# Kernel tuning notes

Measured on AMD Instinct MI355X. Metric: run time of the kernel, lower is better.

The kernel has to match this reference:

```python
import jax, jax.numpy as jnp
import numpy as np

B, N, F_IN = 256, 256, 128
HID, DEPTH = 48, 4
D_OUT = 97                 # sum(latent_dim [32,32,32,1]) = GraphUNet out_channels
K_SORT = 30
C1, C2, KW2 = 16, 32, 5
POOL_LEN = (K_SORT - 2) // 2 + 1        # 15 after maxpool1d(2,2)
DENSE_DIM = (POOL_LEN - KW2 + 1) * C2   # 352
OUT_DIM = 32


def _gcn(x, A, W, b):
    # GCNConv(improved=True): A_hat = A + 2I; out = D^-1/2 A_hat D^-1/2 (x W) + b
    n = A.shape[-1]
    Ah = A + 2.0 * jnp.eye(n, dtype=A.dtype)
    dinv = jax.lax.rsqrt(jnp.sum(Ah, axis=-1))          # deg >= 2 always
    An = dinv[:, :, None] * Ah * dinv[:, None, :]
    return An @ (x @ W) + b


def _augment(A):
    # GraphUNet.augment_adj: add self loops, two-hop (A@A), remove self loops
    n = A.shape[-1]
    eye = jnp.eye(n, dtype=A.dtype)
    A1 = A + eye
    return (A1 @ A1) * (1.0 - eye)


def _topk_pool(x, A, p):
    # TopKPooling(ratio=0.5, nonlinearity=tanh): score = tanh(x.p/||p||)
    Bb, n, _ = x.shape
    score = jnp.tanh((x @ p) / jnp.sqrt(jnp.sum(p * p)))
    k = (n + 1) // 2
    vals, perm = jax.lax.top_k(score, k)                # [B,k]
    bidx = jnp.arange(Bb)[:, None]
    xp = x[bidx, perm] * vals[..., None]                # gate kept nodes by score
    Ap = A[bidx[..., None], perm[:, :, None], perm[:, None, :]]
    return xp, Ap, perm


def _forward(x, A, dW0, db0, dW, db, pool_p, uW, ub, uWl, ubl, c1W, c1b, c2W, c2b, oW, ob):
    act = jax.nn.relu
    # ---- GraphUNet down path ----
    h = act(_gcn(x, A, dW0, db0))
    xs, As, perms = [h], [A], []
    Acur = A
    for i in range(DEPTH):
        A2 = _augment(Acur)
        h, Acur, perm = _topk_pool(h, A2, pool_p[i])
        h = act(_gcn(h, Acur, dW[i], db[i]))
        if i < DEPTH - 1:
            xs.append(h)
            As.append(Acur)
        perms.append(perm)
    # ---- up path with sum skip connections ----
    for i in range(DEPTH):
        j = DEPTH - 1 - i
        res, Aj, perm = xs[j], As[j], perms[j]
        bidx = jnp.arange(res.shape[0])[:, None]
        up = jnp.zeros_like(res).at[bidx, perm].set(h)
        h = res + up
        if i < DEPTH - 1:
            h = act(_gcn(h, Aj, uW[i], ub[i]))
        else:
            h = _gcn(h, Aj, uWl, ubl)                   # [B,N,D_OUT], no act
    # ---- global_sort_pool: sort nodes by last channel desc, keep top K_SORT ----
    _, order = jax.lax.top_k(h[..., -1], K_SORT)
    sp = h[jnp.arange(B)[:, None], order]               # [B,K_SORT,D_OUT]
    # conv1d(1->C1, kernel=stride=D_OUT) on flattened [B,1,K*D] == per-node linear
    y = jax.nn.relu(jnp.einsum('bkd,cd->bck', sp, c1W) + c1b[None, :, None])  # [B,C1,K]
    y = y.reshape(B, C1, POOL_LEN, 2).max(-1)           # maxpool1d(2,2)
    y = jax.lax.conv_general_dilated(y, c2W, (1,), 'VALID',
                                     dimension_numbers=('NCH', 'OIH', 'NCH'))
    y = jax.nn.relu(y + c2b[None, :, None])             # [B,C2,POOL_LEN-KW2+1]
    return jax.nn.relu(y.reshape(B, -1) @ oW + ob)      # relu(relu(.)) == relu(.)


def setup_inputs():
    key = jax.random.key(0)
    ks = jax.random.split(key, 12)
    x = jax.random.normal(ks[0], (B, N, F_IN), dtype=jnp.float32)
    # symmetric binary adjacency, no self loops, avg degree ~15
    u = jax.random.uniform(ks[1], (B, N, N))
    A = (u < 0.03).astype(jnp.float32)
    A = jnp.maximum(A, A.transpose(0, 2, 1)) * (1.0 - jnp.eye(N, dtype=jnp.float32))
    s = lambda f: np.float32(1.0 / np.sqrt(f))
    return dict(
        x=x, A=A,
        dW0=jax.random.normal(ks[2], (F_IN, HID), dtype=jnp.float32) * s(F_IN),
        db0=jnp.zeros((HID,), jnp.float32),
        dW=jax.random.normal(ks[3], (DEPTH, HID, HID), dtype=jnp.float32) * s(HID),
        db=jnp.zeros((DEPTH, HID), jnp.float32),
        pool_p=jax.random.normal(ks[4], (DEPTH, HID), dtype=jnp.float32) * s(HID),
        uW=jax.random.normal(ks[5], (DEPTH - 1, HID, HID), dtype=jnp.float32) * s(HID),
        ub=jnp.zeros((DEPTH - 1, HID), jnp.float32),
        uWl=jax.random.normal(ks[6], (HID, D_OUT), dtype=jnp.float32) * s(HID),
        ubl=jnp.zeros((D_OUT,), jnp.float32),
        c1W=jax.random.normal(ks[7], (C1, D_OUT), dtype=jnp.float32) * s(D_OUT),
        c1b=jnp.zeros((C1,), jnp.float32),
        c2W=jax.random.normal(ks[8], (C2, C1, KW2), dtype=jnp.float32) * s(C1 * KW2),
        c2b=jnp.zeros((C2,), jnp.float32),
        oW=jax.random.normal(ks[9], (DENSE_DIM, OUT_DIM), dtype=jnp.float32) * s(DENSE_DIM),
        ob=jnp.zeros((OUT_DIM,), jnp.float32),
    )


def reference(x, A, dW0, db0, dW, db, pool_p, uW, ub, uWl, ubl, c1W, c1b, c2W, c2b, oW, ob):
    return _forward(x, A, dW0, db0, dW, db, pool_p, uW, ub, uWl, ubl, c1W, c1b, c2W, c2b, oW, ob)
```

## Files before the change

### kernel.cpp

```cpp
#include <hip/hip_runtime.h>
#include <math.h>

#define BATCH 256
#define NNODE 256
#define FIN   128
#define HID   48
#define DOUT  97

#define WOFF_DW0 0
#define WOFF_DW  6144
#define WOFF_UW  18432
#define WOFF_UWL 27648
#define WTOT     34816

typedef __attribute__((ext_vector_type(8))) short bf16x8_t;
typedef __attribute__((ext_vector_type(4))) float f32x4_t;

__device__ inline unsigned short f2bf(float x) {
  unsigned u = __float_as_uint(x);
  u += 0x7fff + ((u >> 16) & 1);
  return (unsigned short)(u >> 16);
}
__device__ inline float bf2f(unsigned short h) {
  return __uint_as_float(((unsigned)h) << 16);
}

template<int L> __device__ inline float grp_sum(float v) {
  #pragma unroll
  for (int o = L >> 1; o > 0; o >>= 1) v += __shfl_xor(v, o);
  return v;
}
template<int L> __device__ inline int grp_isum(int v) {
  #pragma unroll
  for (int o = L >> 1; o > 0; o >>= 1) v += __shfl_xor(v, o);
  return v;
}

__global__ __launch_bounds__(256) void k_prepA(const float* __restrict__ A,
                                               unsigned short* __restrict__ Abf,
                                               float* __restrict__ dinv, int rows) {
  int wid = (blockIdx.x * 256 + threadIdx.x) >> 6;
  int lane = threadIdx.x & 63;
  if (wid >= rows) return;
  const float4* rp = (const float4*)(A + (size_t)wid * 256);
  float4 v = rp[lane];
  unsigned long long pk = (unsigned long long)f2bf(v.x)
                        | ((unsigned long long)f2bf(v.y) << 16)
                        | ((unsigned long long)f2bf(v.z) << 32)
                        | ((unsigned long long)f2bf(v.w) << 48);
  *(unsigned long long*)(Abf + (size_t)wid * 256 + lane * 4) = pk;
  float s = v.x + v.y + v.z + v.w;
  #pragma unroll
  for (int o = 32; o > 0; o >>= 1) s += __shfl_down(s, o);
  if (lane == 0) dinv[wid] = 1.0f / sqrtf(s + 2.0f);
}

__global__ __launch_bounds__(256) void k_dinv_bf(const unsigned short* __restrict__ Abf,
                                                 float* __restrict__ dinv, int n, int rows) {
  int wid = (blockIdx.x * 256 + threadIdx.x) >> 6;
  int lane = threadIdx.x & 63;
  if (wid >= rows) return;
  const unsigned short* row = Abf + (size_t)wid * n;
  float s = 0.f;
  for (int j = lane * 2; j < n; j += 128) {
    unsigned u = *(const unsigned*)(row + j);
    s += bf2f((unsigned short)(u & 0xffffu)) + bf2f((unsigned short)(u >> 16));
  }
  #pragma unroll
  for (int o = 32; o > 0; o >>= 1) s += __shfl_down(s, o);
  if (lane == 0) dinv[wid] = 1.0f / sqrtf(s + 2.0f);
}

__global__ __launch_bounds__(256) void k_splitW3(const float* __restrict__ dW0,
                                                 const float* __restrict__ dW,
                                                 const float* __restrict__ uW,
                                                 const float* __restrict__ uWl,
                                                 unsigned short* __restrict__ Wp) {
  int idx = blockIdx.x * 256 + threadIdx.x;
  if (idx >= WTOT) return;
  float v;
  if (idx < WOFF_DW) {
    int f = idx / 128, kk = idx - f * 128;
    v = dW0[kk * HID + f];
  } else if (idx < WOFF_UW) {
    int r = idx - WOFF_DW;
    int i = r / 3072; r -= i * 3072;
    int f = r / 64, kk = r - f * 64;
    v = (kk < HID) ? dW[((size_t)i * HID + kk) * HID + f] : 0.f;
  } else if (idx < WOFF_UWL) {
    int r = idx - WOFF_UW;
    int i = r / 3072; r -= i * 3072;
    int f = r / 64, kk = r - f * 64;
    v = (kk < HID) ? uW[((size_t)i * HID + kk) * HID + f] : 0.f;
  } else {
    int r = idx - WOFF_UWL;
    int f = r / 64, kk = r - f * 64;
    v = (f < DOUT && kk < HID) ? uWl[(size_t)kk * DOUT + f] : 0.f;
  }
  unsigned short h = f2bf(v);
  float r1 = v - bf2f(h);
  unsigned short m = f2bf(r1);
  float r2 = r1 - bf2f(m);
  unsigned short l = f2bf(r2);
  Wp[idx] = h;
  Wp[idx + WTOT] = m;
  Wp[idx + 2 * WTOT] = l;
}

template<int KS2>
__global__ __launch_bounds__(256) void k_xws(const float* __restrict__ X,
                                             const unsigned short* __restrict__ Wp,
                                             float* __restrict__ XW,
                                             const float* __restrict__ dinv,
                                             unsigned short* __restrict__ Yth,
                                             unsigned short* __restrict__ Ytl,
                                             int K, int F, int Fpad, int nShift) {
  constexpr int KP = KS2 * 32;
  int mt = (blockIdx.x * 256 + threadIdx.x) >> 6;
  int lane = threadIdx.x & 63;
  int r = lane & 15, q = lane >> 4;
  const float* xr = X + ((long)mt * 16 + r) * K;
  bf16x8_t ah[KS2], am[KS2], al[KS2];
  #pragma unroll
  for (int ks = 0; ks < KS2; ks++) {
    int col0 = ks * 32 + q * 8;
    float v[8];
    if (col0 + 8 <= K) {
      float4 a = *(const float4*)(xr + col0);
      float4 b = *(const float4*)(xr + col0 + 4);
      v[0] = a.x; v[1] = a.y; v[2] = a.z; v[3] = a.w;
      v[4] = b.x; v[5] = b.y; v[6] = b.z; v[7] = b.w;
    } else {
      #pragma unroll
      for (int j = 0; j < 8; j++) v[j] = (col0 + j < K) ? xr[col0 + j] : 0.f;
    }
    #pragma unroll
    for (int j = 0; j < 8; j++) {
      unsigned short h = f2bf(v[j]);
      float r1 = v[j] - bf2f(h);
      unsigned short m = f2bf(r1);
      float r2 = r1 - bf2f(m);
      unsigned short l = f2bf(r2);
      ah[ks][j] = (short)h;
      am[ks][j] = (short)m;
      al[ks][j] = (short)l;
    }
  }
  long row0 = (long)mt * 16 + q * 4;
  float4 dv4 = {0.f, 0.f, 0.f, 0.f};
  long ytBase = 0;
  if (Yth) {
    dv4 = *(const float4*)(dinv + row0);
    int bb = (int)(row0 >> nShift);
    int jj = (int)(row0 & ((1 << nShift) - 1));
    ytBase = (long)bb * Fpad;
    ytBase = ytBase << nShift;
    ytBase += jj;
  }
  int nFT = Fpad >> 4;
  for (int ft = 0; ft < nFT; ft++) {
    int fl = ft * 16 + r;
    const unsigned short* wb = Wp + (size_t)fl * KP + q * 8;
    f32x4_t acc = {0.f, 0.f, 0.f, 0.f};
    #pragma unroll
    for (int ks = 0; ks < KS2; ks++) {
      bf16x8_t bh = *(const bf16x8_t*)(wb + ks * 32);
      bf16x8_t bm = *(const bf16x8_t*)(wb + WTOT + ks * 32);
      bf16x8_t bl = *(const bf16x8_t*)(wb + 2 * WTOT + ks * 32);
      acc = __builtin_amdgcn_mfma_f32_16x16x32_bf16(ah[ks], bh, acc, 0, 0, 0);
      acc = __builtin_amdgcn_mfma_f32_16x16x32_bf16(ah[ks], bm, acc, 0, 0, 0);
      acc = __builtin_amdgcn_mfma_f32_16x16x32_bf16(am[ks], bh, acc, 0, 0, 0);
      acc = __builtin_amdgcn_mfma_f32_16x16x32_bf16(am[ks], bm, acc, 0, 0, 0);
      acc = __builtin_amdgcn_mfma_f32_16x16x32_bf16(ah[ks], bl, acc, 0, 0, 0);
      acc = __builtin_amdgcn_mfma_f32_16x16x32_bf16(al[ks], bh, acc, 0, 0, 0);
    }
    int f = fl;
    if (f < F) {
      if (XW) {
        #pragma unroll
        for (int reg = 0; reg < 4; reg++) XW[(row0 + reg) * F + f] = acc[reg];
      }
      if (Yth) {
        float dvv[4] = {dv4.x, dv4.y, dv4.z, dv4.w};
        unsigned long long hpk = 0, lpk = 0;
        #pragma unroll
        for (int reg = 0; reg < 4; reg++) {
          float v = dvv[reg] * acc[reg];
          unsigned short hi = f2bf(v);
          unsigned short lo = f2bf(v - bf2f(hi));
          hpk |= ((unsigned long long)hi) << (16 * reg);
          lpk |= ((unsigned long long)lo) << (16 * reg);
        }
        long o = ytBase + ((long)f << nShift);
        *(unsigned long long*)(Yth + o) = hpk;
        *(unsigned long long*)(Ytl + o) = lpk;
      }
    }
  }
}

template<int KS, int ITP>
__global__ __launch_bounds__(256) void k_gcn2(
    const unsigned short* __restrict__ Abf, const float* __restrict__ dinv,
    const unsigned short* __restrict__ Yth, const unsigned short* __restrict__ Ytl,
    const float* __restrict__ bias, float* __restrict__ out,
    int F, int Fpad, int dorelu) {
  constexpr int n = KS * 32;
  int b = blockIdx.x & (BATCH - 1);
  int sub = blockIdx.x >> 8;
  int wave = threadIdx.x >> 6, lane = threadIdx.x & 63;
  int r = lane & 15, q = lane >> 4;
  const float* dv = dinv + (size_t)b * n;
  int itBase = (sub * 4 + wave) * ITP;
  bf16x8_t af[ITP][KS];
  #pragma unroll
  for (int l = 0; l < ITP; l++) {
    const unsigned short* ap = Abf + ((size_t)b * n + (itBase + l) * 16 + r) * n + q * 8;
    #pragma unroll
    for (int ks = 0; ks < KS; ks++) af[l][ks] = *(const bf16x8_t*)(ap + ks * 32);
  }
  float di[ITP][4];
  #pragma unroll
  for (int l = 0; l < ITP; l++) {
    int i0 = (itBase + l) * 16 + q * 4;
    #pragma unroll
    for (int reg = 0; reg < 4; reg++) di[l][reg] = dv[i0 + reg];
  }
  int nFT = Fpad >> 4;
  for (int ft = 0; ft < nFT; ft++) {
    int fl = ft * 16 + r;
    const unsigned short* yrowh = Yth + ((size_t)b * Fpad + fl) * n;
    const unsigned short* yrowl = Ytl + ((size_t)b * Fpad + fl) * n;
    f32x4_t acc[ITP];
    #pragma unroll
    for (int l = 0; l < ITP; l++) acc[l] = (f32x4_t){0.f, 0.f, 0.f, 0.f};
    #pragma unroll
    for (int ks = 0; ks < KS; ks++) {
      bf16x8_t bh = *(const bf16x8_t*)(yrowh + q * 8 + ks * 32);
      bf16x8_t bl = *(const bf16x8_t*)(yrowl + q * 8 + ks * 32);
      #pragma unroll
      for (int l = 0; l < ITP; l++) {
        acc[l] = __builtin_amdgcn_mfma_f32_16x16x32_bf16(af[l][ks], bh, acc[l], 0, 0, 0);
        acc[l] = __builtin_amdgcn_mfma_f32_16x16x32_bf16(af[l][ks], bl, acc[l], 0, 0, 0);
      }
    }
    if (fl < F) {
      float bf = bias[fl];
      #pragma unroll
      for (int l = 0; l < ITP; l++) {
        int i0 = (itBase + l) * 16 + q * 4;
        unsigned long long hq = *(const unsigned long long*)(yrowh + i0);
        unsigned long long lq = *(const unsigned long long*)(yrowl + i0);
        #pragma unroll
        for (int reg = 0; reg < 4; reg++) {
          float yv = bf2f((unsigned short)(hq >> (16 * reg)))
                   + bf2f((unsigned short)(lq >> (16 * reg)));
          float v = di[l][reg] * acc[l][reg] + 2.f * di[l][reg] * yv + bf;
          if (dorelu) v = fmaxf(v, 0.f);
          out[((size_t)b * n + i0 + reg) * F + fl] = v;
        }
      }
    }
  }
}

__global__ __launch_bounds__(512) void k_htail(const unsigned short* __restrict__ Abf,
                                               const float* __restrict__ dinv,
                                               const unsigned short* __restrict__ Yth,
                                               const unsigned short* __restrict__ Ytl,
                                               const float* __restrict__ ubl,
                                               float* __restrict__ sp) {
  int b = blockIdx.x, t = threadIdx.x;
  __shared__ float sy[256];
  __shared__ float sc[256];
  __shared__ int sord[32];
  const unsigned short* yh = Yth + ((size_t)b * 112 + 96) * 256;
  const unsigned short* yl = Ytl + ((size_t)b * 112 + 96) * 256;
  if (t < 256) sy[t] = bf2f(yh[t]) + bf2f(yl[t]);
  __syncthreads();
  {
    int i = t >> 1, sub = t & 1;
    const unsigned short* ar = Abf + ((size_t)b * 256 + i) * 256 + sub * 128;
    const float* syp = sy + sub * 128;
    float s = 0.f;
    for (int j = 0; j < 128; j += 2) {
      unsigned u = *(const unsigned*)(ar + j);
      s += bf2f((unsigned short)(u & 0xffffu)) * syp[j]
         + bf2f((unsigned short)(u >> 16)) * syp[j + 1];
    }
    s += __shfl_xor(s, 1);
    if (sub == 0) {
      float d = dinv[(size_t)b * 256 + i];
      sc[i] = d * s + 2.f * d * sy[i];
    }
  }
  __syncthreads();
  {
    int i = t >> 1, sub = t & 1;
    float v = sc[i];
    int r = 0;
    int j0 = sub * 128;
    for (int j = j0; j < j0 + 128; j++) {
      float u = sc[j];
      r += (u > v) || (u == v && j < i);
    }
    r += __shfl_xor(r, 1);
    if (sub == 0 && r < 30) sord[r] = i;
  }
  __syncthreads();
  int wave = t >> 6, lane = t & 63;
  int it = wave & 1, fh = wave >> 1;
  int r = lane & 15, q = lane >> 4;
  int ari = it * 16 + r;
  int arow = sord[ari < 30 ? ari : 0];
  const unsigned short* ap = Abf + ((size_t)b * 256 + arow) * 256 + q * 8;
  bf16x8_t af[8];
  #pragma unroll
  for (int ks = 0; ks < 8; ks++) af[ks] = *(const bf16x8_t*)(ap + ks * 32);
  int ftBeg = fh * 2, ftEnd = fh * 2 + 2;
  if (ftEnd > 7) ftEnd = 7;
  for (int ft = ftBeg; ft < ftEnd; ft++) {
    int fl = ft * 16 + r;
    const unsigned short* yrowh = Yth + ((size_t)b * 112 + fl) * 256;
    const unsigned short* yrowl = Ytl + ((size_t)b * 112 + fl) * 256;
    f32x4_t acc = {0.f, 0.f, 0.f, 0.f};
    #pragma unroll
    for (int ks = 0; ks < 8; ks++) {
      bf16x8_t bh = *(const bf16x8_t*)(yrowh + q * 8 + ks * 32);
      bf16x8_t bl = *(const bf16x8_t*)(yrowl + q * 8 + ks * 32);
      acc = __builtin_amdgcn_mfma_f32_16x16x32_bf16(af[ks], bh, acc, 0, 0, 0);
      acc = __builtin_amdgcn_mfma_f32_16x16x32_bf16(af[ks], bl, acc, 0, 0, 0);
    }
    if (fl < DOUT) {
      float bf = ubl[fl];
      #pragma unroll
      for (int reg = 0; reg < 4; reg++) {
        int rowidx = it * 16 + q * 4 + reg;
        if (rowidx < 30) {
          int node = sord[rowidx];
          float d = dinv[(size_t)b * 256 + node];
          float yv = bf2f(yrowh[node]) + bf2f(yrowl[node]);
          sp[((size_t)b * 30 + rowidx) * DOUT + fl] = d * acc[reg] + 2.f * d * yv + bf;
        }
      }
    }
  }
}

__global__ __launch_bounds__(256) void k_aug_mfma(const unsigned short* __restrict__ Abf,
                                                  const int* __restrict__ perm,
                                                  float* __restrict__ Ap,
                                                  unsigned short* __restrict__ Apbf,
                                                  int n, int k) {
  int kt = k >> 4;
  int inner = blockIdx.x & 255;
  int slot = blockIdx.x >> 8;
  int b = ((inner & 7) << 5) | (inner >> 3);
  int wave = threadIdx.x >> 6, lane = threadIdx.x & 63;
  int tile = slot * 4 + wave;
  int it = tile / kt, ft = tile - it * kt;
  int r = lane & 15, q = lane >> 4;
  const int* pm = perm + (size_t)b * k;
  int rowA = pm[it * 16 + r];
  int rowB = pm[ft * 16 + r];
  const unsigned short* Ab = Abf + (size_t)b * n * n;
  const unsigned short* pa = Ab + (size_t)rowA * n + q * 8;
  const unsigned short* pb = Ab + (size_t)rowB * n + q * 8;
  f32x4_t acc = {0.f, 0.f, 0.f, 0.f};
  for (int k0 = 0; k0 < n; k0 += 32) {
    bf16x8_t a  = *(const bf16x8_t*)(pa + k0);
    bf16x8_t bv = *(const bf16x8_t*)(pb + k0);
    int daA = rowA - k0 - q * 8;
    int daB = rowB - k0 - q * 8;
    #pragma unroll
    for (int e = 0; e < 8; e++) {
      if (daA == e) a[e] = (short)0x3F80;
      if (daB == e) bv[e] = (short)0x3F80;
    }
    acc = __builtin_amdgcn_mfma_f32_16x16x32_bf16(a, bv, acc, 0, 0, 0);
  }
  int c = ft * 16 + r;
  #pragma unroll
  for (int reg = 0; reg < 4; reg++) {
    int rr = it * 16 + q * 4 + reg;
    float v = acc[reg];
    if (rr == c) v = 0.f;
    if (Ap)   Ap[((size_t)b * k + rr) * k + c] = v;
    if (Apbf) Apbf[((size_t)b * k + rr) * k + c] = f2bf(v);
  }
}

__global__ __launch_bounds__(256) void k_pool(const float* __restrict__ H,
                                              const float* __restrict__ p,
                                              int* __restrict__ perm,
                                              float* __restrict__ Hout,
                                              int n, int k) {
  int b = blockIdx.x, t = threadIdx.x;
  __shared__ float s[256];
  __shared__ int sord[128];
  float pn = 0.f;
  #pragma unroll
  for (int j = 0; j < HID; j++) pn += p[j] * p[j];
  if (t < n) {
    const float* hr = H + ((size_t)b * n + t) * HID;
    float acc = 0.f;
    #pragma unroll
    for (int j = 0; j < HID; j++) acc += hr[j] * p[j];
    s[t] = tanhf(acc / sqrtf(pn));
  }
  __syncthreads();
  if (t < n) {
    float v = s[t];
    int r = 0;
    for (int j = 0; j < n; j++) {
      float u = s[j];
      r += (u > v) || (u == v && j < t);
    }
    if (r < k) { perm[(size_t)b * k + r] = t; sord[r] = t; }
  }
  __syncthreads();
  for (int idx = t; idx < k * HID; idx += 256) {
    int r = idx / HID, f = idx - r * HID;
    int pi = sord[r];
    Hout[((size_t)b * k + r) * HID + f] = H[((size_t)b * n + pi) * HID + f] * s[pi];
  }
}

__global__ __launch_bounds__(256) void k_scatter(const int* __restrict__ perm,
                                                 const float* __restrict__ Hsrc,
                                                 float* __restrict__ Hdst,
                                                 int n, int k, int total) {
  int idx = blockIdx.x * 256 + threadIdx.x;
  if (idx >= total) return;
  int f = idx % HID;
  int r = (idx / HID) % k;
  int b = idx / (HID * k);
  int pi = perm[(size_t)b * k + r];
  Hdst[((size_t)b * n + pi) * HID + f] += Hsrc[idx];
}

__global__ __launch_bounds__(256) void k_head2(const float* __restrict__ spg,
                                               const float* __restrict__ c1W,
                                               const float* __restrict__ c1b,
                                               const float* __restrict__ c2W,
                                               const float* __restrict__ c2b,
                                               const float* __restrict__ oW,
                                               const float* __restrict__ ob,
                                               float* __restrict__ out) {
  int b = blockIdx.x, t = threadIdx.x;
  __shared__ float sp[30 * 97];
  __shared__ float y1[16 * 30];
  __shared__ float yp[16 * 15];
  __shared__ float yc[32 * 11];
  const float* spb = spg + (size_t)b * 30 * 97;
  for (int idx = t; idx < 30 * 97; idx += 256) sp[idx] = spb[idx];
  __syncthreads();
  for (int idx = t; idx < 16 * 30; idx += 256) {
    int c = idx / 30, kk = idx - c * 30;
    float a = c1b[c];
    for (int d = 0; d < 97; d++) a += sp[kk * 97 + d] * c1W[c * 97 + d];
    y1[c * 30 + kk] = fmaxf(a, 0.f);
  }
  __syncthreads();
  for (int idx = t; idx < 16 * 15; idx += 256) {
    int c = idx / 15, t2 = idx - c * 15;
    yp[idx] = fmaxf(y1[c * 30 + 2 * t2], y1[c * 30 + 2 * t2 + 1]);
  }
  __syncthreads();
  for (int idx = t; idx < 32 * 11; idx += 256) {
    int o = idx / 11, t3 = idx - o * 11;
    float a = c2b[o];
    for (int i2 = 0; i2 < 16; i2++)
      for (int w = 0; w < 5; w++)
        a += yp[i2 * 15 + t3 + w] * c2W[(o * 16 + i2) * 5 + w];
    yc[o * 11 + t3] = fmaxf(a, 0.f);
  }
  __syncthreads();
  if (t < 32) {
    float a = ob[t];
    for (int q = 0; q < 352; q++) a += yc[q] * oW[q * 32 + t];
    out[(size_t)b * 32 + t] = fmaxf(a, 0.f);
  }
}


__device__ inline void xw_dphase(const float* hin, const float* W, const float* dv,
                                 float* xwd, int n, int t) {
  for (int idx = t; idx < n * 48; idx += 512) {
    int j = idx / 48, f = idx - j * 48;
    const float* hr = hin + j * 48;
    float a = 0.f;
    #pragma unroll
    for (int g = 0; g < 48; g++) a += hr[g] * W[g * 48 + f];
    xwd[idx] = dv[j] * a;
  }
}

__device__ inline void anxw_phase(const float* A, int lda, const float* xwd,
                                  const float* dv, const float* bias,
                                  float* hout, int n, int t) {
  for (int idx = t; idx < n * 48; idx += 512) {
    int i = idx / 48, f = idx - i * 48;
    const float* ar = A + i * lda;
    float acc = 0.f;
    #pragma unroll 4
    for (int j = 0; j < n; j++) acc += ar[j] * xwd[j * 48 + f];
    float di = dv[i];
    float v = di * acc + 2.f * di * xwd[i * 48 + f] + bias[f];
    hout[idx] = fmaxf(v, 0.f);
  }
}

template<int N, int K>
__device__ inline void pool_phaseT(const float* h, const float* p,
                                   float* sS, int* perm, float* hin, int t) {
  constexpr int LPR = 512 / N;
  int row = t / LPR, sub = t % LPR;
  float pn = 0.f;
  #pragma unroll
  for (int g = 0; g < 48; g++) pn += p[g] * p[g];
  const float* hr = h + row * 48;
  float acc = 0.f;
  for (int g = sub; g < 48; g += LPR) acc += hr[g] * p[g];
  acc = grp_sum<LPR>(acc);
  if (sub == 0) sS[row] = tanhf(acc / sqrtf(pn));
  __syncthreads();
  {
    float v = sS[row];
    int r = 0;
    for (int j = sub; j < N; j += LPR) {
      float u = sS[j];
      r += (u > v) || (u == v && j < row);
    }
    r = grp_isum<LPR>(r);
    if (sub == 0 && r < K) perm[r] = row;
  }
  __syncthreads();
  for (int idx = t; idx < K * 48; idx += 512) {
    int r = idx / 48, g = idx - r * 48;
    int pi = perm[r];
    hin[idx] = h[pi * 48 + g] * sS[pi];
  }
  __syncthreads();
}

template<int NN, int KK>
__device__ inline void aug_phaseT(const float* A, int lda, const int* perm,
                                  float* Ao, int ldo, float* dout, int t) {
  for (int idx = t; idx < KK * KK; idx += 512) {
    int r = idx / KK, c = idx - r * KK;
    int pr = perm[r], pc = perm[c];
    const float* ra = A + pr * lda;
    const float* rc = A + pc * lda;
    float acc = 0.f;
    #pragma unroll 4
    for (int j = 0; j < NN; j++) acc += ra[j] * rc[j];
    float v = acc + 2.f * ra[pc];
    Ao[r * ldo + c] = (r == c) ? 0.f : v;
  }
  __syncthreads();
  {
    constexpr int LPR = 512 / KK;
    int row = t / LPR, sub = t % LPR;
    float s = 0.f;
    for (int j = sub; j < KK; j += LPR) s += Ao[row * ldo + j];
    s = grp_sum<LPR>(s);
    if (sub == 0) dout[row] = 1.0f / sqrtf(s + 2.0f);
  }
  __syncthreads();
}

__device__ inline void scat_phase(const int* perm, const float* src, float* dst,
                                  int k, int t) {
  for (int idx = t; idx < k * 48; idx += 512) {
    int r = idx / 48, g = idx - r * 48;
    dst[perm[r] * 48 + g] += src[idx];
  }
  __syncthreads();
}

__global__ __launch_bounds__(512) void k_inner(const unsigned short* __restrict__ Abf1g,
                                               float* __restrict__ H1g,
                                               const float* __restrict__ dW,
                                               const float* __restrict__ dbv,
                                               const float* __restrict__ pp,
                                               const float* __restrict__ uW,
                                               const float* __restrict__ ub) {
  int b = blockIdx.x, t = threadIdx.x;
  const unsigned short* A1 = Abf1g + (size_t)b * 128 * 128;
  float* H1 = H1g + (size_t)b * 128 * 48;

  __shared__ float sS[128];
  __shared__ int   sP2[64], sP3[32], sP4[16];
  __shared__ float sD2[64], sD3[32], sD4[16];
  __shared__ float sA2[64 * 65];
  __shared__ float sA3[32 * 33];
  __shared__ float sH2[64 * 48];
  __shared__ float sH3[32 * 48];
  __shared__ float sU[6144];
  float* hin = sU;
  float* sXW = sU + 3072;
  float* sH4 = sU + 1536;
  float* sA4 = sU + 2304;

  {
    const float* p = pp + 48;
    float pn = 0.f;
    #pragma unroll
    for (int g = 0; g < 48; g++) pn += p[g] * p[g];
    int row = t >> 2, sub = t & 3;
    const float* hr = H1 + row * 48;
    float acc = 0.f;
    for (int g = sub; g < 48; g += 4) acc += hr[g] * p[g];
    acc = grp_sum<4>(acc);
    if (sub == 0) sS[row] = tanhf(acc / sqrtf(pn));
    __syncthreads();
    float v = sS[row];
    int rk = 0;
    for (int j = sub; j < 128; j += 4) {
      float u = sS[j];
      rk += (u > v) || (u == v && j < row);
    }
    rk = grp_isum<4>(rk);
    if (sub == 0 && rk < 64) sP2[rk] = row;
    __syncthreads();
  }

  {
    int wave = t >> 6, lane = t & 63;
    int r = lane & 15, q = lane >> 4;
    #pragma unroll
    for (int tt = 0; tt < 2; tt++) {
      int tile = wave * 2 + tt;
      int it = tile >> 2, ft = tile & 3;
      int rowA = sP2[it * 16 + r];
      int rowB = sP2[ft * 16 + r];
      const unsigned short* pa = A1 + (size_t)rowA * 128 + q * 8;
      const unsigned short* pb = A1 + (size_t)rowB * 128 + q * 8;
      f32x4_t acc = {0.f, 0.f, 0.f, 0.f};
      #pragma unroll
      for (int k0 = 0; k0 < 128; k0 += 32) {
        bf16x8_t a  = *(const bf16x8_t*)(pa + k0);
        bf16x8_t bv = *(const bf16x8_t*)(pb + k0);
        int daA = rowA - k0 - q * 8;
        int daB = rowB - k0 - q * 8;
        #pragma unroll
        for (int e = 0; e < 8; e++) {
          if (daA == e) a[e] = (short)0x3F80;
          if (daB == e) bv[e] = (short)0x3F80;
        }
        acc = __builtin_amdgcn_mfma_f32_16x16x32_bf16(a, bv, acc, 0, 0, 0);
      }
      int c = ft * 16 + r;
      #pragma unroll
      for (int reg = 0; reg < 4; reg++) {
        int rr = it * 16 + q * 4 + reg;
        sA2[rr * 65 + c] = (rr == c) ? 0.f : acc[reg];
      }
    }
    for (int idx = t; idx < 64 * 48; idx += 512) {
      int r2 = idx / 48, g = idx - r2 * 48;
      int pi = sP2[r2];
      hin[idx] = H1[pi * 48 + g] * sS[pi];
    }
  }
  __syncthreads();
  {
    int row = t >> 3, sub = t & 7;
    float s = 0.f;
    for (int j = sub; j < 64; j += 8) s += sA2[row * 65 + j];
    s = grp_sum<8>(s);
    if (sub == 0) sD2[row] = 1.0f / sqrtf(s + 2.0f);
  }
  __syncthreads();
  xw_dphase(hin, dW + 2304, sD2, sXW, 64, t);
  __syncthreads();
  anxw_phase(sA2, 65, sXW, sD2, dbv + 48, sH2, 64, t);
  __syncthreads();

  pool_phaseT<64, 32>(sH2, pp + 96, sS, sP3, hin, t);
  aug_phaseT<64, 32>(sA2, 65, sP3, sA3, 33, sD3, t);
  xw_dphase(hin, dW + 2 * 2304, sD3, sXW, 32, t);
  __syncthreads();
  anxw_phase(sA3, 33, sXW, sD3, dbv + 96, sH3, 32, t);
  __syncthreads();

  pool_phaseT<32, 16>(sH3, pp + 144, sS, sP4, hin, t);
  aug_phaseT<32, 16>(sA3, 33, sP4, sA4, 17, sD4, t);
  xw_dphase(hin, dW + 3 * 2304, sD4, sXW, 16, t);
  __syncthreads();
  anxw_phase(sA4, 17, sXW, sD4, dbv + 144, sH4, 16, t);
  __syncthreads();

  scat_phase(sP4, sH4, sH3, 16, t);
  xw_dphase(sH3, uW, sD3, sXW, 32, t);
  __syncthreads();
  anxw_phase(sA3, 33, sXW, sD3, ub, sH3, 32, t);
  __syncthreads();

  scat_phase(sP3, sH3, sH2, 32, t);
  xw_dphase(sH2, uW + 2304, sD2, sXW, 64, t);
  __syncthreads();
  anxw_phase(sA2, 65, sXW, sD2, ub + 48, sH2, 64, t);
  __syncthreads();

  for (int idx = t; idx < 64 * 48; idx += 512) {
    int r2 = idx / 48, g = idx - r2 * 48;
    H1[sP2[r2] * 48 + g] += sH2[idx];
  }
}

extern "C" void kernel_launch(void* const* d_in, const int* in_sizes, int n_in,
                              void* d_out, int out_size, void* d_ws, size_t ws_size,
                              hipStream_t stream) {
  const float* x   = (const float*)d_in[0];
  const float* A0  = (const float*)d_in[1];
  const float* dW0 = (const float*)d_in[2];
  const float* db0 = (const float*)d_in[3];
  const float* dW  = (const float*)d_in[4];
  const float* dbv = (const float*)d_in[5];
  const float* pp  = (const float*)d_in[6];
  const float* uW  = (const float*)d_in[7];
  const float* ub  = (const float*)d_in[8];
  const float* uWl = (const float*)d_in[9];
  const float* ubl = (const float*)d_in[10];
  const float* c1W = (const float*)d_in[11];
  const float* c1b = (const float*)d_in[12];
  const float* c2W = (const float*)d_in[13];
  const float* c2b = (const float*)d_in[14];
  const float* oW  = (const float*)d_in[15];
  const float* ob  = (const float*)d_in[16];
  float* out = (float*)d_out;

  float* base = (float*)d_ws;
  size_t off = 0;
  auto alloc = [&](size_t nel) { nel = (nel + 3) & ~(size_t)3; float* p = base + off; off += nel; return p; };
  float* H0 = alloc((size_t)BATCH * 256 * HID);
  float* H1 = alloc((size_t)BATCH * 128 * HID);
  float* D0 = alloc((size_t)BATCH * 256);
  float* D1 = alloc((size_t)BATCH * 128);
  float* SP  = alloc((size_t)BATCH * 30 * 97);
  int* P1 = (int*)alloc((size_t)BATCH * 128);
  unsigned short* Abf0 = (unsigned short*)alloc((size_t)BATCH * 256 * 256 / 2);
  unsigned short* Abf1 = (unsigned short*)alloc((size_t)BATCH * 128 * 128 / 2);
  unsigned short* Yth  = (unsigned short*)alloc((size_t)BATCH * 112 * 256 / 2);
  unsigned short* Ytl  = (unsigned short*)alloc((size_t)BATCH * 112 * 256 / 2);
  unsigned short* Wp   = (unsigned short*)alloc((size_t)3 * WTOT / 2 + 4);

  k_prepA<<<BATCH * 256 / 4, 256, 0, stream>>>(A0, Abf0, D0, BATCH * 256);
  k_splitW3<<<(WTOT + 255) / 256, 256, 0, stream>>>(dW0, dW, uW, uWl, Wp);

  k_xws<4><<<BATCH * 256 / 64, 256, 0, stream>>>(x, Wp + WOFF_DW0, nullptr,
                                                 D0, Yth, Ytl, FIN, HID, 48, 8);
  k_gcn2<8, 2><<<BATCH * 2, 256, 0, stream>>>(Abf0, D0, Yth, Ytl, db0, H0, HID, 48, 1);

  k_pool<<<BATCH, 256, 0, stream>>>(H0, pp, P1, H1, 256, 128);
  k_aug_mfma<<<16 * 256, 256, 0, stream>>>(Abf0, P1, nullptr, Abf1, 256, 128);
  k_dinv_bf<<<BATCH * 128 / 4, 256, 0, stream>>>(Abf1, D1, 128, BATCH * 128);
  k_xws<2><<<BATCH * 128 / 64, 256, 0, stream>>>(H1, Wp + WOFF_DW, nullptr,
                                                 D1, Yth, Ytl, HID, HID, 48, 7);
  k_gcn2<4, 1><<<BATCH * 2, 256, 0, stream>>>(Abf1, D1, Yth, Ytl, dbv, H1, HID, 48, 1);

  k_inner<<<BATCH, 512, 0, stream>>>(Abf1, H1, dW, dbv, pp, uW, ub);

  k_xws<2><<<BATCH * 128 / 64, 256, 0, stream>>>(H1, Wp + WOFF_UW + 2 * 3072, nullptr,
                                                 D1, Yth, Ytl, HID, HID, 48, 7);
  k_gcn2<4, 1><<<BATCH * 2, 256, 0, stream>>>(Abf1, D1, Yth, Ytl, ub + 2 * HID,
                                              H1, HID, 48, 1);

  k_scatter<<<(BATCH * 128 * HID + 255) / 256, 256, 0, stream>>>(P1, H1, H0,
                                                                 256, 128, BATCH * 128 * HID);
  k_xws<2><<<BATCH * 256 / 64, 256, 0, stream>>>(H0, Wp + WOFF_UWL, nullptr,
                                                 D0, Yth, Ytl, HID, DOUT, 112, 8);
  k_htail<<<BATCH, 512, 0, stream>>>(Abf0, D0, Yth, Ytl, ubl, SP);

  k_head2<<<BATCH, 256, 0, stream>>>(SP, c1W, c1b, c2W, c2b, oW, ob, out);
}
```

Before: 422.6 us.

## Fuse first GCN and mid-level pool/augment/GCN chain into per-graph kernels

Replaces the separate XW, A·XW, pool, augment, degree, inner, GCN and scatter launches with two per-graph 512-thread kernels. The first computes X·W0 into swizzled shared memory and immediately multiplies by A. The second does top-k pooling, two-hop augmentation, the level-1 GCNs, the inner levels and the scatter back to H0 in one block. This removes many launches and global round-trips of Yt, perm and H1 buffers. In exchange, the grid drops to one block per graph with large LDS use, which lowers occupancy.

```diff
diff --git a/kernel.cpp b/kernel.cpp
--- a/kernel.cpp
+++ b/kernel.cpp
@@ -50,22 +50,6 @@
                         | ((unsigned long long)f2bf(v.w) << 48);
   *(unsigned long long*)(Abf + (size_t)wid * 256 + lane * 4) = pk;
   float s = v.x + v.y + v.z + v.w;
-  #pragma unroll
-  for (int o = 32; o > 0; o >>= 1) s += __shfl_down(s, o);
-  if (lane == 0) dinv[wid] = 1.0f / sqrtf(s + 2.0f);
-}
-
-__global__ __launch_bounds__(256) void k_dinv_bf(const unsigned short* __restrict__ Abf,
-                                                 float* __restrict__ dinv, int n, int rows) {
-  int wid = (blockIdx.x * 256 + threadIdx.x) >> 6;
-  int lane = threadIdx.x & 63;
-  if (wid >= rows) return;
-  const unsigned short* row = Abf + (size_t)wid * n;
-  float s = 0.f;
-  for (int j = lane * 2; j < n; j += 128) {
-    unsigned u = *(const unsigned*)(row + j);
-    s += bf2f((unsigned short)(u & 0xffffu)) + bf2f((unsigned short)(u >> 16));
-  }
   #pragma unroll
   for (int o = 32; o > 0; o >>= 1) s += __shfl_down(s, o);
   if (lane == 0) dinv[wid] = 1.0f / sqrtf(s + 2.0f);
@@ -199,69 +183,533 @@
   }
 }
 
-template<int KS, int ITP>
-__global__ __launch_bounds__(256) void k_gcn2(
-    const unsigned short* __restrict__ Abf, const float* __restrict__ dinv,
-    const unsigned short* __restrict__ Yth, const unsigned short* __restrict__ Ytl,
-    const float* __restrict__ bias, float* __restrict__ out,
-    int F, int Fpad, int dorelu) {
-  constexpr int n = KS * 32;
-  int b = blockIdx.x & (BATCH - 1);
-  int sub = blockIdx.x >> 8;
-  int wave = threadIdx.x >> 6, lane = threadIdx.x & 63;
+__global__ __launch_bounds__(512) void k_big(const float* __restrict__ x,
+                                             const unsigned short* __restrict__ Wp0,
+                                             const unsigned short* __restrict__ Abf0,
+                                             const float* __restrict__ D0,
+                                             const float* __restrict__ db0,
+                                             float* __restrict__ H0) {
+  __shared__ __align__(16) char yt0[24576];
+  __shared__ __align__(16) char yt1[24576];
+  int b = blockIdx.x, t = threadIdx.x;
+  int w = t >> 6, lane = t & 63;
   int r = lane & 15, q = lane >> 4;
-  const float* dv = dinv + (size_t)b * n;
-  int itBase = (sub * 4 + wave) * ITP;
-  bf16x8_t af[ITP][KS];
+  const float* Xb = x + (size_t)b * 256 * 128;
+  const float* Db = D0 + (size_t)b * 256;
   #pragma unroll
-  for (int l = 0; l < ITP; l++) {
-    const unsigned short* ap = Abf + ((size_t)b * n + (itBase + l) * 16 + r) * n + q * 8;
-    #pragma unroll
-    for (int ks = 0; ks < KS; ks++) af[l][ks] = *(const bf16x8_t*)(ap + ks * 32);
-  }
-  float di[ITP][4];
+  for (int half = 0; half < 2; half++) {
+    int m = w + half * 8;
+    const float* xr = Xb + (size_t)(m * 16 + r) * 128;
+    bf16x8_t ah[4], am[4], al[4];
+    #pragma unroll
+    for (int ks = 0; ks < 4; ks++) {
+      int col0 = ks * 32 + q * 8;
+      float4 a4 = *(const float4*)(xr + col0);
+      float4 b4 = *(const float4*)(xr + col0 + 4);
+      float v[8] = {a4.x, a4.y, a4.z, a4.w, b4.x, b4.y, b4.z, b4.w};
+      #pragma unroll
+      for (int j = 0; j < 8; j++) {
+        unsigned short h = f2bf(v[j]); float r1 = v[j] - bf2f(h);
+        unsigned short mm = f2bf(r1);  float r2 = r1 - bf2f(mm);
+        ah[ks][j] = (short)h; am[ks][j] = (short)mm; al[ks][j] = (short)f2bf(r2);
+      }
+    }
+    int row0 = m * 16 + q * 4;
+    float4 dv4 = *(const float4*)(Db + row0);
+    float dvv[4] = {dv4.x, dv4.y, dv4.z, dv4.w};
+    #pragma unroll
+    for (int ft = 0; ft < 3; ft++) {
+      int fl = ft * 16 + r;
+      const unsigned short* wb = Wp0 + (size_t)fl * 128 + q * 8;
+      f32x4_t acc = {0.f, 0.f, 0.f, 0.f};
+      #pragma unroll
+      for (int ks = 0; ks < 4; ks++) {
+        bf16x8_t bh = *(const bf16x8_t*)(wb + ks * 32);
+        bf16x8_t bm = *(const bf16x8_t*)(wb + WTOT + ks * 32);
+        bf16x8_t bl = *(const bf16x8_t*)(wb + 2 * WTOT + ks * 32);
+        acc = __builtin_amdgcn_mfma_f32_16x16x32_bf16(ah[ks], bh, acc, 0, 0, 0);
+        acc = __builtin_amdgcn_mfma_f32_16x16x32_bf16(ah[ks], bm, acc, 0, 0, 0);
+        acc = __builtin_amdgcn_mfma_f32_16x16x32_bf16(am[ks], bh, acc, 0, 0, 0);
+        acc = __builtin_amdgcn_mfma_f32_16x16x32_bf16(am[ks], bm, acc, 0, 0, 0);
+        acc = __builtin_amdgcn_mfma_f32_16x16x32_bf16(ah[ks], bl, acc, 0, 0, 0);
+        acc = __builtin_amdgcn_mfma_f32_16x16x32_bf16(al[ks], bh, acc, 0, 0, 0);
+      }
+      #pragma unroll
+      for (int reg = 0; reg < 4; reg++) {
+        float vv = dvv[reg] * acc[reg];
+        unsigned short hi = f2bf(vv);
+        unsigned short lo = f2bf(vv - bf2f(hi));
+        int byte = (fl * 512 + (row0 + reg) * 2) ^ ((fl & 7) << 4);
+        *(unsigned short*)(yt0 + byte) = hi;
+        *(unsigned short*)(yt1 + byte) = lo;
+      }
+    }
+  }
+  __syncthreads();
   #pragma unroll
-  for (int l = 0; l < ITP; l++) {
-    int i0 = (itBase + l) * 16 + q * 4;
-    #pragma unroll
-    for (int reg = 0; reg < 4; reg++) di[l][reg] = dv[i0 + reg];
-  }
-  int nFT = Fpad >> 4;
-  for (int ft = 0; ft < nFT; ft++) {
-    int fl = ft * 16 + r;
-    const unsigned short* yrowh = Yth + ((size_t)b * Fpad + fl) * n;
-    const unsigned short* yrowl = Ytl + ((size_t)b * Fpad + fl) * n;
-    f32x4_t acc[ITP];
-    #pragma unroll
-    for (int l = 0; l < ITP; l++) acc[l] = (f32x4_t){0.f, 0.f, 0.f, 0.f};
-    #pragma unroll
-    for (int ks = 0; ks < KS; ks++) {
-      bf16x8_t bh = *(const bf16x8_t*)(yrowh + q * 8 + ks * 32);
-      bf16x8_t bl = *(const bf16x8_t*)(yrowl + q * 8 + ks * 32);
-      #pragma unroll
-      for (int l = 0; l < ITP; l++) {
-        acc[l] = __builtin_amdgcn_mfma_f32_16x16x32_bf16(af[l][ks], bh, acc[l], 0, 0, 0);
-        acc[l] = __builtin_amdgcn_mfma_f32_16x16x32_bf16(af[l][ks], bl, acc[l], 0, 0, 0);
-      }
-    }
-    if (fl < F) {
-      float bf = bias[fl];
-      #pragma unroll
-      for (int l = 0; l < ITP; l++) {
-        int i0 = (itBase + l) * 16 + q * 4;
-        unsigned long long hq = *(const unsigned long long*)(yrowh + i0);
-        unsigned long long lq = *(const unsigned long long*)(yrowl + i0);
+  for (int half = 0; half < 2; half++) {
+    int it = w + half * 8;
+    const unsigned short* ap = Abf0 + ((size_t)b * 256 + it * 16 + r) * 256 + q * 8;
+    bf16x8_t af[8];
+    #pragma unroll
+    for (int ks = 0; ks < 8; ks++) af[ks] = *(const bf16x8_t*)(ap + ks * 32);
+    #pragma unroll
+    for (int ft = 0; ft < 3; ft++) {
+      int fl = ft * 16 + r;
+      f32x4_t acc = {0.f, 0.f, 0.f, 0.f};
+      #pragma unroll
+      for (int ks = 0; ks < 8; ks++) {
+        int byte = (fl * 512 + (ks * 32 + q * 8) * 2) ^ ((fl & 7) << 4);
+        bf16x8_t bh = *(const bf16x8_t*)(yt0 + byte);
+        bf16x8_t bl = *(const bf16x8_t*)(yt1 + byte);
+        acc = __builtin_amdgcn_mfma_f32_16x16x32_bf16(af[ks], bh, acc, 0, 0, 0);
+        acc = __builtin_amdgcn_mfma_f32_16x16x32_bf16(af[ks], bl, acc, 0, 0, 0);
+      }
+      float bfv = db0[fl];
+      #pragma unroll
+      for (int reg = 0; reg < 4; reg++) {
+        int rr = it * 16 + q * 4 + reg;
+        int sbyte = (fl * 512 + rr * 2) ^ ((fl & 7) << 4);
+        float selfv = bf2f(*(const unsigned short*)(yt0 + sbyte))
+                    + bf2f(*(const unsigned short*)(yt1 + sbyte));
+        float d = Db[rr];
+        float v = d * acc[reg] + 2.f * d * selfv + bfv;
+        H0[((size_t)b * 256 + rr) * 48 + fl] = fmaxf(v, 0.f);
+      }
+    }
+  }
+}
+
+template<int MODE>
+__device__ inline void gcn128_phase(const float* __restrict__ Xg,
+                                    const unsigned short* __restrict__ Wpl,
+                                    const unsigned short* __restrict__ A1,
+                                    const float* __restrict__ D1b,
+                                    const float* __restrict__ bias,
+                                    char* yt0, char* yt1,
+                                    float* __restrict__ H1,
+                                    float* __restrict__ H0b,
+                                    const int* sPerm1, int t) {
+  int w = t >> 6, lane = t & 63;
+  int r = lane & 15, q = lane >> 4;
+  {
+    const float* xr = Xg + (size_t)(w * 16 + r) * 48;
+    bf16x8_t ah[2], am[2], al[2];
+    #pragma unroll
+    for (int ks = 0; ks < 2; ks++) {
+      int col0 = ks * 32 + q * 8;
+      float v[8];
+      if (col0 + 8 <= 48) {
+        float4 a4 = *(const float4*)(xr + col0);
+        float4 b4 = *(const float4*)(xr + col0 + 4);
+        v[0]=a4.x; v[1]=a4.y; v[2]=a4.z; v[3]=a4.w;
+        v[4]=b4.x; v[5]=b4.y; v[6]=b4.z; v[7]=b4.w;
+      } else {
+        #pragma unroll
+        for (int j = 0; j < 8; j++) v[j] = (col0 + j < 48) ? xr[col0 + j] : 0.f;
+      }
+      #pragma unroll
+      for (int j = 0; j < 8; j++) {
+        unsigned short h = f2bf(v[j]); float r1 = v[j] - bf2f(h);
+        unsigned short mm = f2bf(r1);  float r2 = r1 - bf2f(mm);
+        ah[ks][j] = (short)h; am[ks][j] = (short)mm; al[ks][j] = (short)f2bf(r2);
+      }
+    }
+    int row0 = w * 16 + q * 4;
+    float4 dv4 = *(const float4*)(D1b + row0);
+    float dvv[4] = {dv4.x, dv4.y, dv4.z, dv4.w};
+    #pragma unroll
+    for (int ft = 0; ft < 3; ft++) {
+      int fl = ft * 16 + r;
+      const unsigned short* wb = Wpl + (size_t)fl * 64 + q * 8;
+      f32x4_t acc = {0.f, 0.f, 0.f, 0.f};
+      #pragma unroll
+      for (int ks = 0; ks < 2; ks++) {
+        bf16x8_t bh = *(const bf16x8_t*)(wb + ks * 32);
+        bf16x8_t bm = *(const bf16x8_t*)(wb + WTOT + ks * 32);
+        bf16x8_t bl = *(const bf16x8_t*)(wb + 2 * WTOT + ks * 32);
+        acc = __builtin_amdgcn_mfma_f32_16x16x32_bf16(ah[ks], bh, acc, 0, 0, 0);
+        acc = __builtin_amdgcn_mfma_f32_16x16x32_bf16(ah[ks], bm, acc, 0, 0, 0);
+        acc = __builtin_amdgcn_mfma_f32_16x16x32_bf16(am[ks], bh, acc, 0, 0, 0);
+        acc = __builtin_amdgcn_mfma_f32_16x16x32_bf16(am[ks], bm, acc, 0, 0, 0);
+        acc = __builtin_amdgcn_mfma_f32_16x16x32_bf16(ah[ks], bl, acc, 0, 0, 0);
+        acc = __builtin_amdgcn_mfma_f32_16x16x32_bf16(al[ks], bh, acc, 0, 0, 0);
+      }
+      #pragma unroll
+      for (int reg = 0; reg < 4; reg++) {
+        float vv = dvv[reg] * acc[reg];
+        unsigned short hi = f2bf(vv);
+        unsigned short lo = f2bf(vv - bf2f(hi));
+        int byte = (fl * 256 + (row0 + reg) * 2) ^ ((fl & 7) << 4);
+        *(unsigned short*)(yt0 + byte) = hi;
+        *(unsigned short*)(yt1 + byte) = lo;
+      }
+    }
+  }
+  __syncthreads();
+  {
+    const unsigned short* ap = A1 + (size_t)(w * 16 + r) * 128 + q * 8;
+    bf16x8_t af[4];
+    #pragma unroll
+    for (int ks = 0; ks < 4; ks++) af[ks] = *(const bf16x8_t*)(ap + ks * 32);
+    #pragma unroll
+    for (int ft = 0; ft < 3; ft++) {
+      int fl = ft * 16 + r;
+      f32x4_t acc = {0.f, 0.f, 0.f, 0.f};
+      #pragma unroll
+      for (int ks = 0; ks < 4; ks++) {
+        int byte = (fl * 256 + (ks * 32 + q * 8) * 2) ^ ((fl & 7) << 4);
+        bf16x8_t bh = *(const bf16x8_t*)(yt0 + byte);
+        bf16x8_t bl = *(const bf16x8_t*)(yt1 + byte);
+        acc = __builtin_amdgcn_mfma_f32_16x16x32_bf16(af[ks], bh, acc, 0, 0, 0);
+        acc = __builtin_amdgcn_mfma_f32_16x16x32_bf16(af[ks], bl, acc, 0, 0, 0);
+      }
+      float bfv = bias[fl];
+      #pragma unroll
+      for (int reg = 0; reg < 4; reg++) {
+        int rr = w * 16 + q * 4 + reg;
+        int sbyte = (fl * 256 + rr * 2) ^ ((fl & 7) << 4);
+        float selfv = bf2f(*(const unsigned short*)(yt0 + sbyte))
+                    + bf2f(*(const unsigned short*)(yt1 + sbyte));
+        float d = D1b[rr];
+        float v = d * acc[reg] + 2.f * d * selfv + bfv;
+        v = fmaxf(v, 0.f);
+        if (MODE == 0) H1[(size_t)rr * 48 + fl] = v;
+        else {
+          int node = sPerm1[rr];
+          H0b[(size_t)node * 48 + fl] += v;
+        }
+      }
+    }
+  }
+  __syncthreads();
+}
+
+__device__ inline void xw_dphase(const float* hin, const float* W, const float* dv,
+                                 float* xwd, int n, int t) {
+  for (int idx = t; idx < n * 48; idx += 512) {
+    int j = idx / 48, f = idx - j * 48;
+    const float* hr = hin + j * 48;
+    float a = 0.f;
+    #pragma unroll
+    for (int g = 0; g < 48; g++) a += hr[g] * W[g * 48 + f];
+    xwd[idx] = dv[j] * a;
+  }
+}
+
+__device__ inline void anxw_phase(const float* A, int lda, const float* xwd,
+                                  const float* dv, const float* bias,
+                                  float* hout, int n, int t) {
+  for (int idx = t; idx < n * 48; idx += 512) {
+    int i = idx / 48, f = idx - i * 48;
+    const float* ar = A + i * lda;
+    float acc = 0.f;
+    #pragma unroll 4
+    for (int j = 0; j < n; j++) acc += ar[j] * xwd[j * 48 + f];
+    float di = dv[i];
+    float v = di * acc + 2.f * di * xwd[i * 48 + f] + bias[f];
+    hout[idx] = fmaxf(v, 0.f);
+  }
+}
+
+template<int N, int K>
+__device__ inline void pool_phaseT(const float* h, const float* p,
+                                   float* sS, int* perm, float* hin, int t) {
+  constexpr int LPR = 512 / N;
+  int row = t / LPR, sub = t % LPR;
+  float pn = 0.f;
+  #pragma unroll
+  for (int g = 0; g < 48; g++) pn += p[g] * p[g];
+  const float* hr = h + row * 48;
+  float acc = 0.f;
+  for (int g = sub; g < 48; g += LPR) acc += hr[g] * p[g];
+  acc = grp_sum<LPR>(acc);
+  if (sub == 0) sS[row] = tanhf(acc / sqrtf(pn));
+  __syncthreads();
+  {
+    float v = sS[row];
+    int r = 0;
+    for (int j = sub; j < N; j += LPR) {
+      float u = sS[j];
+      r += (u > v) || (u == v && j < row);
+    }
+    r = grp_isum<LPR>(r);
+    if (sub == 0 && r < K) perm[r] = row;
+  }
+  __syncthreads();
+  for (int idx = t; idx < K * 48; idx += 512) {
+    int r = idx / 48, g = idx - r * 48;
+    int pi = perm[r];
+    hin[idx] = h[pi * 48 + g] * sS[pi];
+  }
+  __syncthreads();
+}
+
+template<int NN, int KK>
+__device__ inline void aug_phaseT(const float* A, int lda, const int* perm,
+                                  float* Ao, int ldo, float* dout, int t) {
+  for (int idx = t; idx < KK * KK; idx += 512) {
+    int r = idx / KK, c = idx - r * KK;
+    int pr = perm[r], pc = perm[c];
+    const float* ra = A + pr * lda;
+    const float* rc = A + pc * lda;
+    float acc = 0.f;
+    #pragma unroll 4
+    for (int j = 0; j < NN; j++) acc += ra[j] * rc[j];
+    float v = acc + 2.f * ra[pc];
+    Ao[r * ldo + c] = (r == c) ? 0.f : v;
+  }
+  __syncthreads();
+  {
+    constexpr int LPR = 512 / KK;
+    int row = t / LPR, sub = t % LPR;
+    float s = 0.f;
+    for (int j = sub; j < KK; j += LPR) s += Ao[row * ldo + j];
+    s = grp_sum<LPR>(s);
+    if (sub == 0) dout[row] = 1.0f / sqrtf(s + 2.0f);
+  }
+  __syncthreads();
+}
+
+__device__ inline void scat_phase(const int* perm, const float* src, float* dst,
+                                  int k, int t) {
+  for (int idx = t; idx < k * 48; idx += 512) {
+    int r = idx / 48, g = idx - r * 48;
+    dst[perm[r] * 48 + g] += src[idx];
+  }
+  __syncthreads();
+}
+
+__global__ __launch_bounds__(512) void k_mid(const unsigned short* __restrict__ Abf0,
+                                             unsigned short* __restrict__ Abf1g,
+                                             float* __restrict__ H0,
+                                             float* __restrict__ H1g,
+                                             float* __restrict__ D1g,
+                                             const unsigned short* __restrict__ Wp,
+                                             const float* __restrict__ dW,
+                                             const float* __restrict__ dbv,
+                                             const float* __restrict__ pp,
+                                             const float* __restrict__ uW,
+                                             const float* __restrict__ ub) {
+  int b = blockIdx.x, t = threadIdx.x;
+  __shared__ __align__(16) char arena[63488];
+  __shared__ int sPerm1[128];
+  float* H1 = H1g + (size_t)b * 128 * 48;
+  float* H0b = H0 + (size_t)b * 256 * 48;
+  unsigned short* A1 = Abf1g + (size_t)b * 128 * 128;
+  float* D1b = D1g + (size_t)b * 128;
+
+  {
+    float* sc = (float*)arena;
+    const float* p = pp;
+    float pn = 0.f;
+    #pragma unroll
+    for (int g = 0; g < 48; g++) pn += p[g] * p[g];
+    int row = t >> 1, sub = t & 1;
+    const float* hr = H0b + (size_t)row * 48;
+    float a = 0.f;
+    for (int g = sub; g < 48; g += 2) a += hr[g] * p[g];
+    a = grp_sum<2>(a);
+    if (!sub) sc[row] = tanhf(a / sqrtf(pn));
+    __syncthreads();
+    float vv = sc[row];
+    int rk = 0;
+    for (int j = sub; j < 256; j += 2) {
+      float u = sc[j];
+      rk += (u > vv) || (u == vv && j < row);
+    }
+    rk = grp_isum<2>(rk);
+    if (!sub && rk < 128) sPerm1[rk] = row;
+    __syncthreads();
+    for (int idx = t; idx < 128 * 48; idx += 512) {
+      int rr = idx / 48, g = idx - rr * 48;
+      int pi = sPerm1[rr];
+      H1[idx] = H0b[(size_t)pi * 48 + g] * sc[pi];
+    }
+  }
+  __syncthreads();
+
+  {
+    int w = t >> 6, lane = t & 63;
+    int r = lane & 15, q = lane >> 4;
+    int rowA = sPerm1[w * 16 + r];
+    const unsigned short* Ab = Abf0 + (size_t)b * 256 * 256;
+    const unsigned short* pa = Ab + (size_t)rowA * 256 + q * 8;
+    bf16x8_t af[8];
+    #pragma unroll
+    for (int ks = 0; ks < 8; ks++) {
+      bf16x8_t a = *(const bf16x8_t*)(pa + ks * 32);
+      int da = rowA - ks * 32 - q * 8;
+      #pragma unroll
+      for (int e = 0; e < 8; e++) if (da == e) a[e] = (short)0x3F80;
+      af[ks] = a;
+    }
+    float dsum[4] = {0.f, 0.f, 0.f, 0.f};
+    for (int ft = 0; ft < 8; ft++) {
+      int rowB = sPerm1[ft * 16 + r];
+      const unsigned short* pb = Ab + (size_t)rowB * 256 + q * 8;
+      f32x4_t acc = {0.f, 0.f, 0.f, 0.f};
+      #pragma unroll
+      for (int ks = 0; ks < 8; ks++) {
+        bf16x8_t bv = *(const bf16x8_t*)(pb + ks * 32);
+        int db_ = rowB - ks * 32 - q * 8;
+        #pragma unroll
+        for (int e = 0; e < 8; e++) if (db_ == e) bv[e] = (short)0x3F80;
+        acc = __builtin_amdgcn_mfma_f32_16x16x32_bf16(af[ks], bv, acc, 0, 0, 0);
+      }
+      int c = ft * 16 + r;
+      #pragma unroll
+      for (int reg = 0; reg < 4; reg++) {
+        int rr = w * 16 + q * 4 + reg;
+        float v = (rr == c) ? 0.f : acc[reg];
+        A1[(size_t)rr * 128 + c] = f2bf(v);
+        float s = v;
+        s += __shfl_xor(s, 1); s += __shfl_xor(s, 2);
+        s += __shfl_xor(s, 4); s += __shfl_xor(s, 8);
+        dsum[reg] += s;
+      }
+    }
+    if (r == 0) {
+      #pragma unroll
+      for (int reg = 0; reg < 4; reg++)
+        D1b[w * 16 + q * 4 + reg] = 1.0f / sqrtf(dsum[reg] + 2.0f);
+    }
+  }
+  __syncthreads();
+
+  gcn128_phase<0>(H1, Wp + WOFF_DW, A1, D1b, dbv,
+                  (char*)arena, (char*)arena + 12288, H1, nullptr, sPerm1, t);
+
+  {
+    float* sS  = (float*)(arena);
+    int*   sP2 = (int*)(arena + 512);
+    int*   sP3 = (int*)(arena + 768);
+    int*   sP4 = (int*)(arena + 896);
+    float* sD2 = (float*)(arena + 960);
+    float* sD3 = (float*)(arena + 1216);
+    float* sD4 = (float*)(arena + 1344);
+    float* sA2 = (float*)(arena + 1536);
+    float* sA3 = (float*)(arena + 18176);
+    float* sH2 = (float*)(arena + 22400);
+    float* sH3 = (float*)(arena + 34688);
+    float* sXW = (float*)(arena + 40832);
+    float* hin = (float*)(arena + 53120);
+    float* sH4 = (float*)(arena + 59264);
+    float* sA4 = (float*)(arena + 62336);
+
+    {
+      const float* p = pp + 48;
+      float pn = 0.f;
+      #pragma unroll
+      for (int g = 0; g < 48; g++) pn += p[g] * p[g];
+      int row = t >> 2, sub = t & 3;
+      const float* hr = H1 + (size_t)row * 48;
+      float acc = 0.f;
+      for (int g = sub; g < 48; g += 4) acc += hr[g] * p[g];
+      acc = grp_sum<4>(acc);
+      if (sub == 0) sS[row] = tanhf(acc / sqrtf(pn));
+      __syncthreads();
+      float v = sS[row];
+      int rk = 0;
+      for (int j = sub; j < 128; j += 4) {
+        float u = sS[j];
+        rk += (u > v) || (u == v && j < row);
+      }
+      rk = grp_isum<4>(rk);
+      if (sub == 0 && rk < 64) sP2[rk] = row;
+      __syncthreads();
+    }
+    {
+      int w = t >> 6, lane = t & 63;
+      int r = lane & 15, q = lane >> 4;
+      #pragma unroll
+      for (int tt = 0; tt < 2; tt++) {
+        int tile = w * 2 + tt;
+        int it = tile >> 2, ft = tile & 3;
+        int rowA = sP2[it * 16 + r];
+        int rowB = sP2[ft * 16 + r];
+        const unsigned short* pa = A1 + (size_t)rowA * 128 + q * 8;
+        const unsigned short* pb = A1 + (size_t)rowB * 128 + q * 8;
+        f32x4_t acc = {0.f, 0.f, 0.f, 0.f};
+        #pragma unroll
+        for (int k0 = 0; k0 < 128; k0 += 32) {
+          bf16x8_t a  = *(const bf16x8_t*)(pa + k0);
+          bf16x8_t bv = *(const bf16x8_t*)(pb + k0);
+          int daA = rowA - k0 - q * 8;
+          int daB = rowB - k0 - q * 8;
+          #pragma unroll
+          for (int e = 0; e < 8; e++) {
+            if (daA == e) a[e] = (short)0x3F80;
+            if (daB == e) bv[e] = (short)0x3F80;
+          }
+          acc = __builtin_amdgcn_mfma_f32_16x16x32_bf16(a, bv, acc, 0, 0, 0);
+        }
+        int c = ft * 16 + r;
         #pragma unroll
         for (int reg = 0; reg < 4; reg++) {
-          float yv = bf2f((unsigned short)(hq >> (16 * reg)))
-                   + bf2f((unsigned short)(lq >> (16 * reg)));
-          float v = di[l][reg] * acc[l][reg] + 2.f * di[l][reg] * yv + bf;
-          if (dorelu) v = fmaxf(v, 0.f);
-          out[((size_t)b * n + i0 + reg) * F + fl] = v;
+          int rr = it * 16 + q * 4 + reg;
+          sA2[rr * 65 + c] = (rr == c) ? 0.f : acc[reg];
         }
       }
     }
-  }
+    __syncthreads();
+    {
+      int row = t >> 3, sub = t & 7;
+      float s = 0.f;
+      for (int j = sub; j < 64; j += 8) s += sA2[row * 65 + j];
+      s = grp_sum<8>(s);
+      if (sub == 0) sD2[row] = 1.0f / sqrtf(s + 2.0f);
+    }
+    __syncthreads();
+    for (int idx = t; idx < 64 * 48; idx += 512) {
+      int j = idx / 48, f = idx - j * 48;
+      int pi = sP2[j];
+      const float* hr = H1 + (size_t)pi * 48;
+      const float* W = dW + 2304;
+      float a = 0.f;
+      #pragma unroll
+      for (int g = 0; g < 48; g++) a += hr[g] * W[g * 48 + f];
+      sXW[idx] = sD2[j] * sS[pi] * a;
+    }
+    __syncthreads();
+    anxw_phase(sA2, 65, sXW, sD2, dbv + 48, sH2, 64, t);
+    __syncthreads();
+
+    pool_phaseT<64, 32>(sH2, pp + 96, sS, sP3, hin, t);
+    aug_phaseT<64, 32>(sA2, 65, sP3, sA3, 33, sD3, t);
+    xw_dphase(hin, dW + 2 * 2304, sD3, sXW, 32, t);
+    __syncthreads();
+    anxw_phase(sA3, 33, sXW, sD3, dbv + 96, sH3, 32, t);
+    __syncthreads();
+
+    pool_phaseT<32, 16>(sH3, pp + 144, sS, sP4, hin, t);
+    aug_phaseT<32, 16>(sA3, 33, sP4, sA4, 17, sD4, t);
+    xw_dphase(hin, dW + 3 * 2304, sD4, sXW, 16, t);
+    __syncthreads();
+    anxw_phase(sA4, 17, sXW, sD4, dbv + 144, sH4, 16, t);
+    __syncthreads();
+
+    scat_phase(sP4, sH4, sH3, 16, t);
+    xw_dphase(sH3, uW, sD3, sXW, 32, t);
+    __syncthreads();
+    anxw_phase(sA3, 33, sXW, sD3, ub, sH3, 32, t);
+    __syncthreads();
+
+    scat_phase(sP3, sH3, sH2, 32, t);
+    xw_dphase(sH2, uW + 2304, sD2, sXW, 64, t);
+    __syncthreads();
+    anxw_phase(sA2, 65, sXW, sD2, ub + 48, sH2, 64, t);
+    __syncthreads();
+
+    for (int idx = t; idx < 64 * 48; idx += 512) {
+      int r2 = idx / 48, g = idx - r2 * 48;
+      H1[(size_t)sP2[r2] * 48 + g] += sH2[idx];
+    }
+  }
+  __syncthreads();
+
+  gcn128_phase<1>(H1, Wp + WOFF_UW + 2 * 3072, A1, D1b, ub + 96,
+                  (char*)arena, (char*)arena + 12288, nullptr, H0b, sPerm1, t);
 }
 
 __global__ __launch_bounds__(512) void k_htail(const unsigned short* __restrict__ Abf,
@@ -347,98 +795,6 @@
   }
 }
 
-__global__ __launch_bounds__(256) void k_aug_mfma(const unsigned short* __restrict__ Abf,
-                                                  const int* __restrict__ perm,
-                                                  float* __restrict__ Ap,
-                                                  unsigned short* __restrict__ Apbf,
-                                                  int n, int k) {
-  int kt = k >> 4;
-  int inner = blockIdx.x & 255;
-  int slot = blockIdx.x >> 8;
-  int b = ((inner & 7) << 5) | (inner >> 3);
-  int wave = threadIdx.x >> 6, lane = threadIdx.x & 63;
-  int tile = slot * 4 + wave;
-  int it = tile / kt, ft = tile - it * kt;
-  int r = lane & 15, q = lane >> 4;
-  const int* pm = perm + (size_t)b * k;
-  int rowA = pm[it * 16 + r];
-  int rowB = pm[ft * 16 + r];
-  const unsigned short* Ab = Abf + (size_t)b * n * n;
-  const unsigned short* pa = Ab + (size_t)rowA * n + q * 8;
-  const unsigned short* pb = Ab + (size_t)rowB * n + q * 8;
-  f32x4_t acc = {0.f, 0.f, 0.f, 0.f};
-  for (int k0 = 0; k0 < n; k0 += 32) {
-    bf16x8_t a  = *(const bf16x8_t*)(pa + k0);
-    bf16x8_t bv = *(const bf16x8_t*)(pb + k0);
-    int daA = rowA - k0 - q * 8;
-    int daB = rowB - k0 - q * 8;
-    #pragma unroll
-    for (int e = 0; e < 8; e++) {
-      if (daA == e) a[e] = (short)0x3F80;
-      if (daB == e) bv[e] = (short)0x3F80;
-    }
-    acc = __builtin_amdgcn_mfma_f32_16x16x32_bf16(a, bv, acc, 0, 0, 0);
-  }
-  int c = ft * 16 + r;
-  #pragma unroll
-  for (int reg = 0; reg < 4; reg++) {
-    int rr = it * 16 + q * 4 + reg;
-    float v = acc[reg];
-    if (rr == c) v = 0.f;
-    if (Ap)   Ap[((size_t)b * k + rr) * k + c] = v;
-    if (Apbf) Apbf[((size_t)b * k + rr) * k + c] = f2bf(v);
-  }
-}
-
-__global__ __launch_bounds__(256) void k_pool(const float* __restrict__ H,
-                                              const float* __restrict__ p,
-                                              int* __restrict__ perm,
-                                              float* __restrict__ Hout,
-                                              int n, int k) {
-  int b = blockIdx.x, t = threadIdx.x;
-  __shared__ float s[256];
-  __shared__ int sord[128];
-  float pn = 0.f;
-  #pragma unroll
-  for (int j = 0; j < HID; j++) pn += p[j] * p[j];
-  if (t < n) {
-    const float* hr = H + ((size_t)b * n + t) * HID;
-    float acc = 0.f;
-    #pragma unroll
-    for (int j = 0; j < HID; j++) acc += hr[j] * p[j];
-    s[t] = tanhf(acc / sqrtf(pn));
-  }
-  __syncthreads();
-  if (t < n) {
-    float v = s[t];
-    int r = 0;
-    for (int j = 0; j < n; j++) {
-      float u = s[j];
-      r += (u > v) || (u == v && j < t);
-    }
-    if (r < k) { perm[(size_t)b * k + r] = t; sord[r] = t; }
-  }
-  __syncthreads();
-  for (int idx = t; idx < k * HID; idx += 256) {
-    int r = idx / HID, f = idx - r * HID;
-    int pi = sord[r];
-    Hout[((size_t)b * k + r) * HID + f] = H[((size_t)b * n + pi) * HID + f] * s[pi];
-  }
-}
-
-__global__ __launch_bounds__(256) void k_scatter(const int* __restrict__ perm,
-                                                 const float* __restrict__ Hsrc,
-                                                 float* __restrict__ Hdst,
-                                                 int n, int k, int total) {
-  int idx = blockIdx.x * 256 + threadIdx.x;
-  if (idx >= total) return;
-  int f = idx % HID;
-  int r = (idx / HID) % k;
-  int b = idx / (HID * k);
-  int pi = perm[(size_t)b * k + r];
-  Hdst[((size_t)b * n + pi) * HID + f] += Hsrc[idx];
-}
-
 __global__ __launch_bounds__(256) void k_head2(const float* __restrict__ spg,
                                                const float* __restrict__ c1W,
                                                const float* __restrict__ c1b,
@@ -452,6 +808,7 @@
   __shared__ float y1[16 * 30];
   __shared__ float yp[16 * 15];
   __shared__ float yc[32 * 11];
+  __shared__ float red[256];
   const float* spb = spg + (size_t)b * 30 * 97;
   for (int idx = t; idx < 30 * 97; idx += 256) sp[idx] = spb[idx];
   __syncthreads();
@@ -476,237 +833,18 @@
     yc[o * 11 + t3] = fmaxf(a, 0.f);
   }
   __syncthreads();
+  {
+    int o = t & 31, g = t >> 5;
+    float a = 0.f;
+    for (int qq = g * 44; qq < g * 44 + 44; qq++) a += yc[qq] * oW[qq * 32 + o];
+    red[t] = a;
+  }
+  __syncthreads();
   if (t < 32) {
     float a = ob[t];
-    for (int q = 0; q < 352; q++) a += yc[q] * oW[q * 32 + t];
+    #pragma unroll
+    for (int g = 0; g < 8; g++) a += red[t + 32 * g];
     out[(size_t)b * 32 + t] = fmaxf(a, 0.f);
-  }
-}
-
-
-__device__ inline void xw_dphase(const float* hin, const float* W, const float* dv,
-                                 float* xwd, int n, int t) {
-  for (int idx = t; idx < n * 48; idx += 512) {
-    int j = idx / 48, f = idx - j * 48;
-    const float* hr = hin + j * 48;
-    float a = 0.f;
-    #pragma unroll
-    for (int g = 0; g < 48; g++) a += hr[g] * W[g * 48 + f];
-    xwd[idx] = dv[j] * a;
-  }
-}
-
-__device__ inline void anxw_phase(const float* A, int lda, const float* xwd,
-                                  const float* dv, const float* bias,
-                                  float* hout, int n, int t) {
-  for (int idx = t; idx < n * 48; idx += 512) {
-    int i = idx / 48, f = idx - i * 48;
-    const float* ar = A + i * lda;
-    float acc = 0.f;
-    #pragma unroll 4
-    for (int j = 0; j < n; j++) acc += ar[j] * xwd[j * 48 + f];
-    float di = dv[i];
-    float v = di * acc + 2.f * di * xwd[i * 48 + f] + bias[f];
-    hout[idx] = fmaxf(v, 0.f);
-  }
-}
-
-template<int N, int K>
-__device__ inline void pool_phaseT(const float* h, const float* p,
-                                   float* sS, int* perm, float* hin, int t) {
-  constexpr int LPR = 512 / N;
-  int row = t / LPR, sub = t % LPR;
-  float pn = 0.f;
-  #pragma unroll
-  for (int g = 0; g < 48; g++) pn += p[g] * p[g];
-  const float* hr = h + row * 48;
-  float acc = 0.f;
-  for (int g = sub; g < 48; g += LPR) acc += hr[g] * p[g];
-  acc = grp_sum<LPR>(acc);
-  if (sub == 0) sS[row] = tanhf(acc / sqrtf(pn));
-  __syncthreads();
-  {
-    float v = sS[row];
-    int r = 0;
-    for (int j = sub; j < N; j += LPR) {
-      float u = sS[j];
-      r += (u > v) || (u == v && j < row);
-    }
-    r = grp_isum<LPR>(r);
-    if (sub == 0 && r < K) perm[r] = row;
-  }
-  __syncthreads();
-  for (int idx = t; idx < K * 48; idx += 512) {
-    int r = idx / 48, g = idx - r * 48;
-    int pi = perm[r];
-    hin[idx] = h[pi * 48 + g] * sS[pi];
-  }
-  __syncthreads();
-}
-
-template<int NN, int KK>
-__device__ inline void aug_phaseT(const float* A, int lda, const int* perm,
-                                  float* Ao, int ldo, float* dout, int t) {
-  for (int idx = t; idx < KK * KK; idx += 512) {
-    int r = idx / KK, c = idx - r * KK;
-    int pr = perm[r], pc = perm[c];
-    const float* ra = A + pr * lda;
-    const float* rc = A + pc * lda;
-    float acc = 0.f;
-    #pragma unroll 4
-    for (int j = 0; j < NN; j++) acc += ra[j] * rc[j];
-    float v = acc + 2.f * ra[pc];
-    Ao[r * ldo + c] = (r == c) ? 0.f : v;
-  }
-  __syncthreads();
-  {
-    constexpr int LPR = 512 / KK;
-    int row = t / LPR, sub = t % LPR;
-    float s = 0.f;
-    for (int j = sub; j < KK; j += LPR) s += Ao[row * ldo + j];
-    s = grp_sum<LPR>(s);
-    if (sub == 0) dout[row] = 1.0f / sqrtf(s + 2.0f);
-  }
-  __syncthreads();
-}
-
-__device__ inline void scat_phase(const int* perm, const float* src, float* dst,
-                                  int k, int t) {
-  for (int idx = t; idx < k * 48; idx += 512) {
-    int r = idx / 48, g = idx - r * 48;
-    dst[perm[r] * 48 + g] += src[idx];
-  }
-  __syncthreads();
-}
-
-__global__ __launch_bounds__(512) void k_inner(const unsigned short* __restrict__ Abf1g,
-                                               float* __restrict__ H1g,
-                                               const float* __restrict__ dW,
-                                               const float* __restrict__ dbv,
-                                               const float* __restrict__ pp,
-                                               const float* __restrict__ uW,
-                                               const float* __restrict__ ub) {
-  int b = blockIdx.x, t = threadIdx.x;
-  const unsigned short* A1 = Abf1g + (size_t)b * 128 * 128;
-  float* H1 = H1g + (size_t)b * 128 * 48;
-
-  __shared__ float sS[128];
-  __shared__ int   sP2[64], sP3[32], sP4[16];
-  __shared__ float sD2[64], sD3[32], sD4[16];
-  __shared__ float sA2[64 * 65];
-  __shared__ float sA3[32 * 33];
-  __shared__ float sH2[64 * 48];
-  __shared__ float sH3[32 * 48];
-  __shared__ float sU[6144];
-  float* hin = sU;
-  float* sXW = sU + 3072;
-  float* sH4 = sU + 1536;
-  float* sA4 = sU + 2304;
-
-  {
-    const float* p = pp + 48;
-    float pn = 0.f;
-    #pragma unroll
-    for (int g = 0; g < 48; g++) pn += p[g] * p[g];
-    int row = t >> 2, sub = t & 3;
-    const float* hr = H1 + row * 48;
-    float acc = 0.f;
-    for (int g = sub; g < 48; g += 4) acc += hr[g] * p[g];
-    acc = grp_sum<4>(acc);
-    if (sub == 0) sS[row] = tanhf(acc / sqrtf(pn));
-    __syncthreads();
-    float v = sS[row];
-    int rk = 0;
-    for (int j = sub; j < 128; j += 4) {
-      float u = sS[j];
-      rk += (u > v) || (u == v && j < row);
-    }
-    rk = grp_isum<4>(rk);
-    if (sub == 0 && rk < 64) sP2[rk] = row;
-    __syncthreads();
-  }
-
-  {
-    int wave = t >> 6, lane = t & 63;
-    int r = lane & 15, q = lane >> 4;
-    #pragma unroll
-    for (int tt = 0; tt < 2; tt++) {
-      int tile = wave * 2 + tt;
-      int it = tile >> 2, ft = tile & 3;
-      int rowA = sP2[it * 16 + r];
-      int rowB = sP2[ft * 16 + r];
-      const unsigned short* pa = A1 + (size_t)rowA * 128 + q * 8;
-      const unsigned short* pb = A1 + (size_t)rowB * 128 + q * 8;
-      f32x4_t acc = {0.f, 0.f, 0.f, 0.f};
-      #pragma unroll
-      for (int k0 = 0; k0 < 128; k0 += 32) {
-        bf16x8_t a  = *(const bf16x8_t*)(pa + k0);
-        bf16x8_t bv = *(const bf16x8_t*)(pb + k0);
-        int daA = rowA - k0 - q * 8;
-        int daB = rowB - k0 - q * 8;
-        #pragma unroll
-        for (int e = 0; e < 8; e++) {
-          if (daA == e) a[e] = (short)0x3F80;
-          if (daB == e) bv[e] = (short)0x3F80;
-        }
-        acc = __builtin_amdgcn_mfma_f32_16x16x32_bf16(a, bv, acc, 0, 0, 0);
-      }
-      int c = ft * 16 + r;
-      #pragma unroll
-      for (int reg = 0; reg < 4; reg++) {
-        int rr = it * 16 + q * 4 + reg;
-        sA2[rr * 65 + c] = (rr == c) ? 0.f : acc[reg];
-      }
-    }
-    for (int idx = t; idx < 64 * 48; idx += 512) {
-      int r2 = idx / 48, g = idx - r2 * 48;
-      int pi = sP2[r2];
-      hin[idx] = H1[pi * 48 + g] * sS[pi];
-    }
-  }
-  __syncthreads();
-  {
-    int row = t >> 3, sub = t & 7;
-    float s = 0.f;
-    for (int j = sub; j < 64; j += 8) s += sA2[row * 65 + j];
-    s = grp_sum<8>(s);
-    if (sub == 0) sD2[row] = 1.0f / sqrtf(s + 2.0f);
-  }
-  __syncthreads();
-  xw_dphase(hin, dW + 2304, sD2, sXW, 64, t);
-  __syncthreads();
-  anxw_phase(sA2, 65, sXW, sD2, dbv + 48, sH2, 64, t);
-  __syncthreads();
-
-  pool_phaseT<64, 32>(sH2, pp + 96, sS, sP3, hin, t);
-  aug_phaseT<64, 32>(sA2, 65, sP3, sA3, 33, sD3, t);
-  xw_dphase(hin, dW + 2 * 2304, sD3, sXW, 32, t);
-  __syncthreads();
-  anxw_phase(sA3, 33, sXW, sD3, dbv + 96, sH3, 32, t);
-  __syncthreads();
-
-  pool_phaseT<32, 16>(sH3, pp + 144, sS, sP4, hin, t);
-  aug_phaseT<32, 16>(sA3, 33, sP4, sA4, 17, sD4, t);
-  xw_dphase(hin, dW + 3 * 2304, sD4, sXW, 16, t);
-  __syncthreads();
-  anxw_phase(sA4, 17, sXW, sD4, dbv + 144, sH4, 16, t);
-  __syncthreads();
-
-  scat_phase(sP4, sH4, sH3, 16, t);
-  xw_dphase(sH3, uW, sD3, sXW, 32, t);
-  __syncthreads();
-  anxw_phase(sA3, 33, sXW, sD3, ub, sH3, 32, t);
-  __syncthreads();
-
-  scat_phase(sP3, sH3, sH2, 32, t);
-  xw_dphase(sH2, uW + 2304, sD2, sXW, 64, t);
-  __syncthreads();
-  anxw_phase(sA2, 65, sXW, sD2, ub + 48, sH2, 64, t);
-  __syncthreads();
-
-  for (int idx = t; idx < 64 * 48; idx += 512) {
-    int r2 = idx / 48, g = idx - r2 * 48;
-    H1[sP2[r2] * 48 + g] += sH2[idx];
   }
 }
 
@@ -739,8 +877,7 @@
   float* H1 = alloc((size_t)BATCH * 128 * HID);
   float* D0 = alloc((size_t)BATCH * 256);
   float* D1 = alloc((size_t)BATCH * 128);
-  float* SP  = alloc((size_t)BATCH * 30 * 97);
-  int* P1 = (int*)alloc((size_t)BATCH * 128);
+  float* SP = alloc((size_t)BATCH * 30 * 97);
   unsigned short* Abf0 = (unsigned short*)alloc((size_t)BATCH * 256 * 256 / 2);
   unsigned short* Abf1 = (unsigned short*)alloc((size_t)BATCH * 128 * 128 / 2);
   unsigned short* Yth  = (unsigned short*)alloc((size_t)BATCH * 112 * 256 / 2);
@@ -750,26 +887,10 @@
   k_prepA<<<BATCH * 256 / 4, 256, 0, stream>>>(A0, Abf0, D0, BATCH * 256);
   k_splitW3<<<(WTOT + 255) / 256, 256, 0, stream>>>(dW0, dW, uW, uWl, Wp);
 
-  k_xws<4><<<BATCH * 256 / 64, 256, 0, stream>>>(x, Wp + WOFF_DW0, nullptr,
-                                                 D0, Yth, Ytl, FIN, HID, 48, 8);
-  k_gcn2<8, 2><<<BATCH * 2, 256, 0, stream>>>(Abf0, D0, Yth, Ytl, db0, H0, HID, 48, 1);
-
-  k_pool<<<BATCH, 256, 0, stream>>>(H0, pp, P1, H1, 256, 128);
-  k_aug_mfma<<<16 * 256, 256, 0, stream>>>(Abf0, P1, nullptr, Abf1, 256, 128);
-  k_dinv_bf<<<BATCH * 128 / 4, 256, 0, stream>>>(Abf1, D1, 128, BATCH * 128);
-  k_xws<2><<<BATCH * 128 / 64, 256, 0, stream>>>(H1, Wp + WOFF_DW, nullptr,
-                                                 D1, Yth, Ytl, HID, HID, 48, 7);
-  k_gcn2<4, 1><<<BATCH * 2, 256, 0, stream>>>(Abf1, D1, Yth, Ytl, dbv, H1, HID, 48, 1);
-
-  k_inner<<<BATCH, 512, 0, stream>>>(Abf1, H1, dW, dbv, pp, uW, ub);
-
-  k_xws<2><<<BATCH * 128 / 64, 256, 0, stream>>>(H1, Wp + WOFF_UW + 2 * 3072, nullptr,
-                                                 D1, Yth, Ytl, HID, HID, 48, 7);
-  k_gcn2<4, 1><<<BATCH * 2, 256, 0, stream>>>(Abf1, D1, Yth, Ytl, ub + 2 * HID,
-                                              H1, HID, 48, 1);
-
-  k_scatter<<<(BATCH * 128 * HID + 255) / 256, 256, 0, stream>>>(P1, H1, H0,
-                                                                 256, 128, BATCH * 128 * HID);
+  k_big<<<BATCH, 512, 0, stream>>>(x, Wp + WOFF_DW0, Abf0, D0, db0, H0);
+
+  k_mid<<<BATCH, 512, 0, stream>>>(Abf0, Abf1, H0, H1, D1, Wp, dW, dbv, pp, uW, ub);
+
   k_xws<2><<<BATCH * 256 / 64, 256, 0, stream>>>(H0, Wp + WOFF_UWL, nullptr,
                                                  D0, Yth, Ytl, HID, DOUT, 112, 8);
   k_htail<<<BATCH, 512, 0, stream>>>(Abf0, D0, Yth, Ytl, ubl, SP);
```

After: 423.6 us. Within noise of the previous version (+0.2%).
